# Performance work log

Measured on AMD Instinct MI355X. Metric: run time of the kernel, lower is better.

The kernel has to match this reference:

```python
import jax, jax.numpy as jnp
import numpy as np

V, K, D, T, B, M = 32000, 32, 256, 128, 128, 16
NEG = -1e9


def setup_inputs():
    key = jax.random.key(0)
    ks = jax.random.split(key, 32)
    def rn(k, shape):
        return (0.05 * jax.random.normal(k, shape)).astype(jnp.float32)
    u = jax.random.uniform(ks[4], (T, B, K), minval=1e-6, maxval=1.0 - 1e-6)
    return dict(
        keys=jax.random.randint(ks[0], (B, M), 1, V),
        vals=jax.random.randint(ks[1], (B, M), 1, V),
        sentences=jax.random.randint(ks[2], (B, T), 1, V),
        sent_lens=jax.random.randint(ks[3], (B,), T // 2, T + 1),
        tau=jnp.float32(0.5),
        x_lambd=jnp.float32(0.5),
        gumbel_noise=(-jnp.log(-jnp.log(u))).astype(jnp.float32),
        drop_unif=jax.random.uniform(ks[5], (B, T)).astype(jnp.float32),
        emb=rn(ks[6], (V, D)), z_emb=rn(ks[7], (K, D)),
        enc_Wih=rn(ks[8], (D, 4 * D)), enc_Whh=rn(ks[9], (D, 4 * D)), enc_b=jnp.zeros((4 * D,), jnp.float32),
        crf_W=rn(ks[10], (D, K)), crf_b=jnp.zeros((K,), jnp.float32), crf_trans=rn(ks[11], (K, K)),
        init_Wh=rn(ks[12], (D, D)), init_bh=jnp.zeros((D,), jnp.float32),
        init_Wc=rn(ks[13], (D, D)), init_bc=jnp.zeros((D,), jnp.float32),
        dec_Wih=rn(ks[14], (D, 4 * D)), dec_Whh=rn(ks[15], (D, 4 * D)), dec_b=jnp.zeros((4 * D,), jnp.float32),
        attn_Wq=rn(ks[16], (D, D)), attn_Wk=rn(ks[17], (D, D)), attn_v=rn(ks[18], (D,)),
        attn_out_W=rn(ks[19], (2 * D, D)), attn_out_b=jnp.zeros((D,), jnp.float32),
        pz_W=rn(ks[20], (D, K)), pz_b=jnp.zeros((K,), jnp.float32),
        int_W=rn(ks[21], (2 * D, D)), int_b=jnp.zeros((D,), jnp.float32),
        out_W=rn(ks[22], (D, V)), out_b=jnp.zeros((V,), jnp.float32),
        cattn_Wq=rn(ks[23], (D, D)), cattn_Wk=rn(ks[24], (D, D)), cattn_v=rn(ks[25], (D,)),
        g_W=rn(ks[26], (D, 1)), g_b=jnp.zeros((1,), jnp.float32),
    )


def _lstm_step(h, c, x, Wih, Whh, b):
    g = x @ Wih + h @ Whh + b
    i, f, gg, o = jnp.split(g, 4, axis=-1)
    c = jax.nn.sigmoid(f) * c + jax.nn.sigmoid(i) * jnp.tanh(gg)
    h = jax.nn.sigmoid(o) * jnp.tanh(c)
    return h, c


def _attend(q, memk, mem_vals, mask, v):
    # additive attention: q [B,D], memk = mem @ Wk [B,M,D]
    e = jnp.einsum('bmd,d->bm', jnp.tanh(q[:, None, :] + memk), v)
    e = jnp.where(mask, e, NEG)
    a = jax.nn.softmax(e, axis=-1)
    ctx = jnp.einsum('bm,bmd->bd', a, mem_vals)
    return ctx, a


def _forward(tau, x_lambd, gumbel_noise, drop_unif, emb, z_emb,
             enc_Wih, enc_Whh, enc_b, crf_W, crf_b, crf_trans,
             init_Wh, init_bh, init_Wc, init_bc,
             dec_Wih, dec_Whh, dec_b,
             attn_Wq, attn_Wk, attn_v, attn_out_W, attn_out_b,
             pz_W, pz_b, int_W, int_b, out_W, out_b,
             cattn_Wq, cattn_Wk, cattn_v, g_W, g_b,
             keys, vals, sentences, sent_lens):
    z_beta = 1.0
    lens = sent_lens
    # ---- q encoder: 1-layer LSTM over sentence embeddings ----
    sent_emb = emb[sentences]                            # [B,T,D]
    def enc_step(carry, x_t):
        h, c = _lstm_step(carry[0], carry[1], x_t, enc_Wih, enc_Whh, enc_b)
        return (h, c), h
    z0 = jnp.zeros((B, D), jnp.float32)
    _, enc_out = jax.lax.scan(enc_step, (z0, z0), sent_emb.transpose(1, 0, 2))
    enc_out = enc_out.transpose(1, 0, 2)                 # [B,T,D]
    # ---- emission scores with overlap logits ----
    phi = enc_out @ crf_W + crf_b                        # [B,T,K]
    phi = phi.at[:, :-1].add(phi[:, 1:])                 # scores[:,:-1] += scores[:,1:].clone()
    phi = phi.at[:, 1:].add(phi[:, :-1])                 # scores[:,1:]  += scores[:,:-1].clone()
    # ---- linear-chain CRF forward recursion: alpha + exact entropy ----
    phiT = phi.transpose(1, 0, 2)                        # [T,B,K]
    def crf_step(carry, inputs):
        alpha, H = carry
        phi_t, t = inputs
        scores = alpha[:, :, None] + crf_trans[None]     # [B,Ki,Kj]
        lZ = jax.nn.logsumexp(scores, axis=1)            # [B,Kj]
        logw = scores - lZ[:, None, :]
        w = jnp.exp(logw)
        na = lZ + phi_t
        nH = jnp.sum(w * (H[:, :, None] - logw), axis=1)
        m = (t < lens)[:, None]
        na = jnp.where(m, na, alpha)
        nH = jnp.where(m, nH, H)
        return (na, nH), na
    (aT, HT), alphas = jax.lax.scan(
        crf_step, (phiT[0], jnp.zeros((B, K), jnp.float32)),
        (phiT[1:], jnp.arange(1, T)))
    alphas = jnp.concatenate([phiT[0][None], alphas], axis=0)   # [T,B,K]
    logp_last = jax.nn.log_softmax(aT, axis=-1)
    ent_z = jnp.mean(jnp.sum(jnp.exp(logp_last) * (HT - logp_last), axis=-1))
    # ---- Gumbel FFBS backward sampling ----
    def bwd_step(nid, inputs):
        alpha_t, g_t, t = inputs
        is_last = (t == lens - 1)[:, None]
        active = (t < lens)
        logits = jnp.where(is_last, alpha_t, alpha_t + crf_trans[:, nid].T)
        y = jax.nn.softmax((logits + g_t) / tau, axis=-1)
        y = jnp.where(active[:, None], y, 0.0)
        ids = jnp.where(active, jnp.argmax(y, axis=-1).astype(jnp.int32), 0)
        return ids, (ids, y)
    ts = jnp.arange(T)
    _, (ids_r, y_r) = jax.lax.scan(
        bwd_step, jnp.zeros((B,), jnp.int32),
        (alphas[::-1], gumbel_noise[::-1], ts[::-1]))
    z_ids = ids_r[::-1].transpose(1, 0)                  # [B,T]
    z_sample = y_r[::-1].transpose(1, 0, 2)              # [B,T,K]
    z_sample_emb = z_sample @ z_emb                      # soft gumbel encode [B,T,D]
    # ---- key-value table encoding ----
    kv_mask = keys != 0
    kv_emb = emb[keys] + emb[vals]                       # [B,M,D]
    kvm = kv_mask.astype(jnp.float32)
    kv_enc = (kv_emb * kvm[..., None]).sum(1) / kvm.sum(1, keepdims=True)
    # ---- decoder io (word dropout x_lambd, z[0] zeroed) ----
    zse = z_sample_emb.at[:, 0].multiply(0.0)
    wmask = (drop_unif > x_lambd).astype(jnp.float32)[..., None]
    dec_inputs = (zse + sent_emb * wmask)[:, :-1]        # [B,T-1,D]
    tgt_x = sentences[:, 1:]
    tgt_z = z_ids[:, 1:]
    z_next = z_sample_emb[:, 1:]
    h0 = kv_enc @ init_Wh + init_bh
    c0 = kv_enc @ init_Wc + init_bc
    memk = kv_emb @ attn_Wk
    memk2 = kv_emb @ cattn_Wk
    rows = jnp.arange(B)
    def dec_step(carry, inputs):
        h, c = carry
        x_t, zn_t, tx, tz = inputs
        h, c = _lstm_step(h, c, x_t, dec_Wih, dec_Whh, dec_b)
        ctx, _ = _attend(h @ attn_Wq, memk, kv_emb, kv_mask, attn_v)
        dec_out = jnp.concatenate([h, ctx], axis=-1) @ attn_out_W + attn_out_b
        z_logits = dec_out @ pz_W + pz_b
        lpz = jnp.take_along_axis(jax.nn.log_softmax(z_logits, -1), tz[:, None], 1)[:, 0]
        dec_int = jnp.concatenate([dec_out, zn_t], axis=-1) @ int_W + int_b
        lm_prob = jax.nn.softmax(dec_int @ out_W + out_b, axis=-1)       # [B,V]
        _, copy_dist = _attend(dec_int @ cattn_Wq, memk2, kv_emb, kv_mask, cattn_v)
        copy_prob = jnp.zeros((B, V), lm_prob.dtype).at[rows[:, None], keys].add(copy_dist)
        g = jax.nn.sigmoid(dec_int @ g_W + g_b)                           # [B,1]
        out_prob = (1.0 - g) * lm_prob + g * copy_prob
        lpx = jnp.log(jnp.take_along_axis(out_prob, tx[:, None], 1)[:, 0] + 1e-10)
        return (h, c), (lpx, lpz)
    _, (lpx, lpz) = jax.lax.scan(
        dec_step, (h0, c0),
        (dec_inputs.transpose(1, 0, 2), z_next.transpose(1, 0, 2),
         tgt_x.transpose(1, 0), tgt_z.transpose(1, 0)))
    steps = jnp.arange(T - 1)
    smask = (steps[None, :] < lens[:, None]).astype(jnp.float32)
    denom = jnp.sum(lens).astype(jnp.float32)
    p_log_prob = (jnp.sum(lpx.transpose(1, 0) * smask) + jnp.sum(lpz.transpose(1, 0) * smask)) / denom
    loss = -(z_beta * ent_z + p_log_prob)
    return loss


def reference(keys, vals, sentences, sent_lens, tau, x_lambd, gumbel_noise,
              drop_unif, emb, z_emb, enc_Wih, enc_Whh, enc_b, crf_W, crf_b,
              crf_trans, init_Wh, init_bh, init_Wc, init_bc, dec_Wih, dec_Whh,
              dec_b, attn_Wq, attn_Wk, attn_v, attn_out_W, attn_out_b, pz_W,
              pz_b, int_W, int_b, out_W, out_b, cattn_Wq, cattn_Wk, cattn_v,
              g_W, g_b):
    return _forward(tau, x_lambd, gumbel_noise, drop_unif, emb, z_emb,
                    enc_Wih, enc_Whh, enc_b, crf_W, crf_b, crf_trans,
                    init_Wh, init_bh, init_Wc, init_bc, dec_Wih, dec_Whh,
                    dec_b, attn_Wq, attn_Wk, attn_v, attn_out_W, attn_out_b,
                    pz_W, pz_b, int_W, int_b, out_W, out_b,
                    cattn_Wq, cattn_Wk, cattn_v, g_W, g_b,
                    keys, vals, sentences, sent_lens)
```

## Files before the change

kernel.cpp:

```cpp
#include <hip/hip_runtime.h>
#include <math.h>

namespace {

constexpr int V_  = 32000;
constexpr int K_  = 32;
constexpr int D_  = 256;
constexpr int T_  = 128;
constexpr int B_  = 128;
constexpr int M_  = 16;
constexpr int D4_ = 1024;
constexpr int TD_ = T_ - 1;
constexpr int R_  = B_ * TD_;
constexpr int NCH_ = 8;

typedef __attribute__((ext_vector_type(8))) short short8;
typedef __attribute__((ext_vector_type(4))) float f32x4;
typedef __attribute__((ext_vector_type(2))) float f32x2;

__device__ __forceinline__ float d_rcp(float x){
#if __has_builtin(__builtin_amdgcn_rcpf)
  return __builtin_amdgcn_rcpf(x);
#else
  return 1.0f / x;
#endif
}
__device__ __forceinline__ float d_sig(float x){
  return d_rcp(1.0f + __expf(-x));
}
__device__ __forceinline__ float d_tanh(float x){
  float e = __expf(2.0f*x);
  return 1.0f - 2.0f*d_rcp(e + 1.0f);
}
__device__ __forceinline__ unsigned short f2bf(float f){
  unsigned int x = __float_as_uint(f);
  unsigned int r = (x + 0x7FFFu + ((x>>16)&1u)) >> 16;
  return (unsigned short)r;
}

__device__ __forceinline__ unsigned f2fp8(float f){
  unsigned u = __float_as_uint(f);
  unsigned s = (u>>31)<<7;
  float a = fabsf(f);
  if (a < 0.015625f){
    int m = (int)rintf(a*512.0f);
    if (m >= 8) return s | 0x08u;
    return s | (unsigned)m;
  }
  unsigned t = u & 0x7FFFFFFFu;
  t += 0x7FFFFu + ((t>>20)&1u);
  int E = (int)(t>>23) - 127 + 7;
  if (E >= 16) return s | 0x7Eu;
  return s | ((unsigned)E<<3) | ((t>>20)&7u);
}

__device__ __forceinline__ unsigned pack4_fp8(float a, float b, float c, float d){
#if __has_builtin(__builtin_amdgcn_cvt_pk_fp8_f32)
  unsigned r = (unsigned)__builtin_amdgcn_cvt_pk_fp8_f32(a, b, 0, false);
  r = (unsigned)__builtin_amdgcn_cvt_pk_fp8_f32(c, d, (int)r, true);
  return r;
#else
  return f2fp8(a) | (f2fp8(b)<<8) | (f2fp8(c)<<16) | (f2fp8(d)<<24);
#endif
}
__device__ __forceinline__ unsigned char f2fp8_b(float f){
#if __has_builtin(__builtin_amdgcn_cvt_pk_fp8_f32)
  return (unsigned char)(__builtin_amdgcn_cvt_pk_fp8_f32(f, f, 0, false) & 0xFF);
#else
  return (unsigned char)f2fp8(f);
#endif
}

__device__ __forceinline__ void cvt4_fp8(unsigned w, float* o){
#if __has_builtin(__builtin_amdgcn_cvt_pk_f32_fp8)
  f32x2 lo = __builtin_amdgcn_cvt_pk_f32_fp8(w, false);
  f32x2 hi = __builtin_amdgcn_cvt_pk_f32_fp8(w, true);
  o[0]=lo.x; o[1]=lo.y; o[2]=hi.x; o[3]=hi.y;
#else
  #pragma unroll
  for (int j = 0; j < 4; j++){
    unsigned b = (w>>(8*j)) & 0xFFu;
    unsigned e = (b>>3) & 15u, m = b & 7u;
    float mag = e ? __uint_as_float(((e+120u)<<23)|(m<<20)) : (float)m*0.001953125f;
    o[j] = (b & 0x80u) ? -mag : mag;
  }
#endif
}

__global__ void k_emb2(const int* __restrict__ sent, const int* __restrict__ keys,
                       const int* __restrict__ vals, const float* __restrict__ emb,
                       float* __restrict__ sent_emb, float* __restrict__ kv){
  int bid = blockIdx.x, tid = threadIdx.x;
  if (bid < B_*T_){
    sent_emb[(size_t)bid*256 + tid] = emb[(size_t)sent[bid]*D_ + tid];
  } else {
    int r = bid - B_*T_;
    kv[(size_t)r*256 + tid] = emb[(size_t)keys[r]*D_ + tid]
                            + emb[(size_t)vals[r]*D_ + tid];
  }
}

__global__ void k_kv_enc(const int* __restrict__ keys, const float* __restrict__ kv,
                         float* __restrict__ out){
  int idx = blockIdx.x*256 + threadIdx.x;
  int b = idx >> 8, d = idx & 255;
  float s = 0.0f, c = 0.0f;
  for (int m = 0; m < M_; m++){
    if (keys[b*M_+m] != 0){ s += kv[(size_t)(b*M_+m)*D_ + d]; c += 1.0f; }
  }
  out[idx] = s / c;
}

__global__ void k_rowgemm(const float* __restrict__ A, const float* __restrict__ W,
                          const float* __restrict__ bias, float* __restrict__ C,
                          int inner, int cols){
  __shared__ float sA[256];
  int r = blockIdx.x;
  if ((int)threadIdx.x < inner) sA[threadIdx.x] = A[(size_t)r*inner + threadIdx.x];
  __syncthreads();
  for (int j = threadIdx.x; j < cols; j += blockDim.x){
    float acc = bias ? bias[j] : 0.0f;
    #pragma unroll 4
    for (int d = 0; d < inner; d++) acc += sA[d]*W[(size_t)d*cols + j];
    C[(size_t)r*cols + j] = acc;
  }
}

__global__ void k_rowgemm2(const float* __restrict__ A,
                           const float* __restrict__ W1, const float* __restrict__ b1,
                           float* __restrict__ C1,
                           const float* __restrict__ W2, const float* __restrict__ b2,
                           float* __restrict__ C2, int inner, int cols){
  __shared__ float sA[256];
  int r = blockIdx.x;
  if ((int)threadIdx.x < inner) sA[threadIdx.x] = A[(size_t)r*inner + threadIdx.x];
  __syncthreads();
  for (int j = threadIdx.x; j < cols; j += blockDim.x){
    float a1 = b1 ? b1[j] : 0.0f;
    float a2 = b2 ? b2[j] : 0.0f;
    #pragma unroll 4
    for (int d = 0; d < inner; d++){
      float a = sA[d];
      a1 += a*W1[(size_t)d*cols + j];
      a2 += a*W2[(size_t)d*cols + j];
    }
    C1[(size_t)r*cols + j] = a1;
    C2[(size_t)r*cols + j] = a2;
  }
}

__global__ __launch_bounds__(256) void k_wt8(const float* __restrict__ W,
                                             unsigned char* __restrict__ Wt8, int ldw){
  __shared__ unsigned char st[64][272];
  int tid = threadIdx.x; size_t c0 = (size_t)blockIdx.x*64;
  for (int l = tid; l < 64*256; l += 256){
    int k = l >> 6, c = l & 63;
    st[c][k] = f2fp8_b(W[(size_t)k*ldw + c0 + c]);
  }
  __syncthreads();
  for (int l = tid; l < 64*16; l += 256){
    int c = l >> 4, s = l & 15;
    *reinterpret_cast<uint4*>(&Wt8[(c0+c)*256 + s*16]) =
      *reinterpret_cast<const uint4*>(&st[c][s*16]);
  }
}

__global__ __launch_bounds__(256) void k_wt8_2(const float* __restrict__ W1,
    const float* __restrict__ W2, unsigned char* __restrict__ O1,
    unsigned char* __restrict__ O2, int ldw){
  __shared__ unsigned char st[64][272];
  const float* W = (blockIdx.x < 16) ? W1 : W2;
  unsigned char* O = (blockIdx.x < 16) ? O1 : O2;
  int tid = threadIdx.x; size_t c0 = (size_t)(blockIdx.x & 15)*64;
  for (int l = tid; l < 64*256; l += 256){
    int k = l >> 6, c = l & 63;
    st[c][k] = f2fp8_b(W[(size_t)k*ldw + c0 + c]);
  }
  __syncthreads();
  for (int l = tid; l < 64*16; l += 256){
    int c = l >> 4, s = l & 15;
    *reinterpret_cast<uint4*>(&O[(c0+c)*256 + s*16]) =
      *reinterpret_cast<const uint4*>(&st[c][s*16]);
  }
}

__global__ __launch_bounds__(256) void k_wtg2(const float* __restrict__ W1,
    const float* __restrict__ W2, unsigned short* __restrict__ O1,
    unsigned short* __restrict__ O2, int ldw){
  __shared__ unsigned short st[64][264];
  const float* W = (blockIdx.x < 16) ? W1 : W2;
  unsigned short* O = (blockIdx.x < 16) ? O1 : O2;
  int tid = threadIdx.x; size_t c0 = (size_t)(blockIdx.x & 15)*64;
  for (int l = tid; l < 64*256; l += 256){
    int k = l >> 6, c = l & 63;
    st[c][k] = f2bf(W[(size_t)k*ldw + c0 + c]);
  }
  __syncthreads();
  for (int l = tid; l < 64*32; l += 256){
    int c = l >> 5, s = l & 31;
    *reinterpret_cast<uint4*>(&O[(c0+c)*256 + s*8]) =
      *reinterpret_cast<const uint4*>(&st[c][s*8]);
  }
}

__global__ __launch_bounds__(256) void k_wtg6(
    const float* s0, const float* s1, const float* s2,
    const float* s3, const float* s4, const float* s5,
    unsigned short* d0, unsigned short* d1, unsigned short* d2,
    unsigned short* d3, unsigned short* d4, unsigned short* d5){
  __shared__ unsigned short st[64][264];
  int m = blockIdx.x >> 2, blk = blockIdx.x & 3;
  const float* S; unsigned short* D;
  if      (m == 0){ S = s0; D = d0; }
  else if (m == 1){ S = s1; D = d1; }
  else if (m == 2){ S = s2; D = d2; }
  else if (m == 3){ S = s3; D = d3; }
  else if (m == 4){ S = s4; D = d4; }
  else            { S = s5; D = d5; }
  int tid = threadIdx.x; size_t c0 = (size_t)blk*64;
  for (int l = tid; l < 64*256; l += 256){
    int k = l >> 6, c = l & 63;
    st[c][k] = f2bf(S[(size_t)k*256 + c0 + c]);
  }
  __syncthreads();
  for (int l = tid; l < 64*32; l += 256){
    int c = l >> 5, s = l & 31;
    *reinterpret_cast<uint4*>(&D[(c0+c)*256 + s*8]) =
      *reinterpret_cast<const uint4*>(&st[c][s*8]);
  }
}

template<int G1, int G2, int HALVES, int CPB, bool BIAS, int TMD>
__global__ __launch_bounds__(512) void k_gemm(
    const float* __restrict__ A1, const float* __restrict__ A2,
    const unsigned short* __restrict__ W1, const unsigned short* __restrict__ W2,
    const float* __restrict__ bias, float* __restrict__ C, int cols,
    const float* __restrict__ drop, const float* __restrict__ xl){
  __shared__ unsigned short Al[128*256];
  __shared__ unsigned short Wl[64*256];
  int tid = threadIdx.x;
  int row0 = blockIdx.x*128;
  int w = tid >> 6, l = tid & 63;
  int arow = 16*w + (l & 15);
  float xlv = 0.0f;
  if constexpr (G1==1) xlv = xl[0];
  f32x4 acc[CPB][4];
  #pragma unroll
  for (int cc=0;cc<CPB;cc++)
    #pragma unroll
    for (int nf=0;nf<4;nf++) acc[cc][nf] = (f32x4){0.f,0.f,0.f,0.f};

  for (int h = 0; h < HALVES; h++){
    const float* Asrc = h ? A2 : A1;
    const unsigned short* Wt = h ? W2 : W1;
    int gm = h ? G2 : G1;
    __syncthreads();
    #pragma unroll
    for (int q = 0; q < 8; q++){
      int u = tid + q*512;
      int row = u >> 5, slot = u & 31;
      int r = row0 + row;
      float vals[8];
      if (gm == 0){
        const float* s = Asrc + (size_t)r*256 + slot*8;
        #pragma unroll
        for (int j=0;j<8;j++) vals[j] = s[j];
      } else if (gm == 1){
        int b = r / TD_, t = r - b*TD_;
        int bt = b*T_ + t;
        float wm = (drop[bt] > xlv) ? 1.0f : 0.0f;
        const float* se = A1 + (size_t)bt*256 + slot*8;
        const float* zs = A2 + (size_t)bt*256 + slot*8;
        #pragma unroll
        for (int j=0;j<8;j++) vals[j] = se[j]*wm + (t>0 ? zs[j] : 0.0f);
      } else {
        int b = r / TD_, t = r - b*TD_;
        const float* s = Asrc + (size_t)(b*T_ + t + 1)*256 + slot*8;
        #pragma unroll
        for (int j=0;j<8;j++) vals[j] = s[j];
      }
      union { unsigned short us[8]; uint4 v4; } tu;
      #pragma unroll
      for (int j=0;j<8;j++) tu.us[j] = f2bf(vals[j]);
      int dst = row*512 + ((slot*16) ^ ((row&7)<<4));
      *reinterpret_cast<uint4*>(reinterpret_cast<char*>(Al) + dst) = tu.v4;
    }
    __syncthreads();
    short8 afr[8];
    #pragma unroll
    for (int k0 = 0; k0 < 8; k0++){
      int kb = k0*64 + ((l>>4)*16);
      afr[k0] = *reinterpret_cast<const short8*>(
          reinterpret_cast<const char*>(Al) + arow*512 + (kb ^ ((arow&7)<<4)));
    }
    for (int cc = 0; cc < CPB; cc++){
      int col0 = (blockIdx.y*CPB + cc)*64;
      __syncthreads();
      #pragma unroll
      for (int q = 0; q < 4; q++){
        int u = tid + q*512;
        int c = u >> 5, slot = u & 31;
        int dst = c*512 + ((slot*16) ^ ((c&7)<<4));
        *reinterpret_cast<uint4*>(reinterpret_cast<char*>(Wl) + dst) =
          *reinterpret_cast<const uint4*>(
              reinterpret_cast<const char*>(Wt) + (size_t)(col0+c)*512 + slot*16);
      }
      __syncthreads();
      #pragma unroll
      for (int k0 = 0; k0 < 8; k0++){
        int kb = k0*64 + ((l>>4)*16);
        #pragma unroll
        for (int nf = 0; nf < 4; nf++){
          int bc = nf*16 + (l & 15);
          short8 bfr = *reinterpret_cast<const short8*>(
              reinterpret_cast<const char*>(Wl) + bc*512 + (kb ^ ((bc&7)<<4)));
          acc[cc][nf] = __builtin_amdgcn_mfma_f32_16x16x32_bf16(afr[k0], bfr, acc[cc][nf], 0, 0, 0);
        }
      }
    }
  }
  #pragma unroll
  for (int cc = 0; cc < CPB; cc++){
    int col0 = (blockIdx.y*CPB + cc)*64;
    #pragma unroll
    for (int nf = 0; nf < 4; nf++){
      int col = col0 + nf*16 + (l & 15);
      float bv = BIAS ? bias[col] : 0.0f;
      #pragma unroll
      for (int r4 = 0; r4 < 4; r4++){
        int row = row0 + 16*w + (l>>4)*4 + r4;
        size_t orow;
        if constexpr (TMD == 0){
          orow = (size_t)row;
        } else {
          int bb = row / TMD, tt = row - bb*TMD;
          orow = (size_t)tt*B_ + bb;
        }
        C[orow*cols + col] = acc[cc][nf][r4] + bv;
      }
    }
  }
}

__global__ __launch_bounds__(1024, 4) void k_lstm12(
    const float* __restrict__ xW,
    const unsigned char* __restrict__ Wt,
    const float* __restrict__ h0, const float* __restrict__ c0,
    float* __restrict__ Hout,
    int NT){
  __shared__ unsigned char Wl[512*256];
  __shared__ unsigned char Ahl[2][16*256];
  int g0 = blockIdx.x;
  int tid = threadIdx.x;
  int w = tid >> 6, l = tid & 63;

  for (int i = tid; i < 512*16; i += 1024){
    int c = i >> 4, s16 = i & 15;
    int dst = c*256 + ((s16*16) ^ ((c&7)<<4));
    *reinterpret_cast<uint4*>(&Wl[dst]) =
      *reinterpret_cast<const uint4*>(&Wt[(size_t)c*256 + s16*16]);
  }
  if (tid < 256){
    int row = tid >> 4, gblk = tid & 15;
    unsigned pk[4];
    #pragma unroll
    for (int g = 0; g < 4; g++){
      float v0 = h0 ? h0[(size_t)(g0*16+row)*256 + gblk*16 + 4*g + 0] : 0.0f;
      float v1 = h0 ? h0[(size_t)(g0*16+row)*256 + gblk*16 + 4*g + 1] : 0.0f;
      float v2 = h0 ? h0[(size_t)(g0*16+row)*256 + gblk*16 + 4*g + 2] : 0.0f;
      float v3 = h0 ? h0[(size_t)(g0*16+row)*256 + gblk*16 + 4*g + 3] : 0.0f;
      pk[g] = pack4_fp8(v0, v1, v2, v3);
    }
    int dst = row*256 + ((gblk*16) ^ ((row&7)<<4));
    *reinterpret_cast<uint4*>(&Ahl[0][dst]) = *reinterpret_cast<const uint4*>(pk);
  }
  int cb = 16*w + (l & 15);
  int arow = l & 15;
  float creg[4];
  #pragma unroll
  for (int r = 0; r < 4; r++)
    creg[r] = c0 ? c0[(size_t)(g0*16 + (l>>4)*4 + r)*256 + cb] : 0.0f;

  int aoff[8], b0off[8], b1off[8];
  #pragma unroll
  for (int k0 = 0; k0 < 8; k0++){
    int kb = k0*32 + ((l>>4)*8);
    aoff[k0]  = arow*256 + (kb ^ ((arow&7)<<4));
    b0off[k0] = cb*256 + (kb ^ ((cb&7)<<4));
    b1off[k0] = (256+cb)*256 + (kb ^ ((cb&7)<<4));
  }
  const unsigned char* wg2 = Wt + (size_t)(512+cb)*256 + ((l>>4)*8);
  const unsigned char* wg3 = Wt + (size_t)(768+cb)*256 + ((l>>4)*8);
  int astore[4];
  const float* xb[4];
  float* hp[4];
  #pragma unroll
  for (int r = 0; r < 4; r++){
    int batch = (l>>4)*4 + r;
    astore[r] = batch*256 + ((cb & 0xF0) ^ ((batch&7)<<4)) + (cb & 15);
    xb[r] = xW + (size_t)(g0*16 + batch)*1024 + cb;
    hp[r] = Hout + (size_t)(g0*16 + batch)*NT*256 + cb;
  }
  __syncthreads();

  float xn[4][4];
  #pragma unroll
  for (int gt = 0; gt < 4; gt++)
    #pragma unroll
    for (int r = 0; r < 4; r++)
      xn[gt][r] = xb[r][gt*256];

  for (int t = 0; t < NT; t++){
    int cur = t & 1, nxt = cur ^ 1;
    f32x4 acc[4];
    #pragma unroll
    for (int gt = 0; gt < 4; gt++)
      #pragma unroll
      for (int r = 0; r < 4; r++)
        acc[gt][r] = xn[gt][r];
    if (t + 1 < NT){
      #pragma unroll
      for (int r = 0; r < 4; r++) xb[r] += B_*1024;
      #pragma unroll
      for (int gt = 0; gt < 4; gt++)
        #pragma unroll
        for (int r = 0; r < 4; r++)
          xn[gt][r] = xb[r][gt*256];
    }
    const unsigned char* Ac = Ahl[cur];
    #pragma unroll
    for (int k0 = 0; k0 < 8; k0++){
      long long afr = *reinterpret_cast<const long long*>(Ac + aoff[k0]);
      long long b0 = *reinterpret_cast<const long long*>(Wl + b0off[k0]);
      long long b1 = *reinterpret_cast<const long long*>(Wl + b1off[k0]);
      long long b2 = *reinterpret_cast<const long long*>(wg2 + k0*32);
      long long b3 = *reinterpret_cast<const long long*>(wg3 + k0*32);
      acc[0] = __builtin_amdgcn_mfma_f32_16x16x32_fp8_fp8(afr, b0, acc[0], 0, 0, 0);
      acc[1] = __builtin_amdgcn_mfma_f32_16x16x32_fp8_fp8(afr, b1, acc[1], 0, 0, 0);
      acc[2] = __builtin_amdgcn_mfma_f32_16x16x32_fp8_fp8(afr, b2, acc[2], 0, 0, 0);
      acc[3] = __builtin_amdgcn_mfma_f32_16x16x32_fp8_fp8(afr, b3, acc[3], 0, 0, 0);
    }
    #pragma unroll
    for (int r = 0; r < 4; r++){
      float vi = acc[0][r], vf = acc[1][r];
      float vg = acc[2][r], vo = acc[3][r];
      float cn = d_sig(vf)*creg[r] + d_sig(vi)*d_tanh(vg);
      float hn = d_sig(vo)*d_tanh(cn);
      creg[r] = cn;
      Ahl[nxt][astore[r]] = f2fp8_b(hn);
      hp[r][0] = hn;
      hp[r] += 256;
    }
    __syncthreads();
  }
}

__global__ __launch_bounds__(256) void k_phi(const float* __restrict__ H,
    const float* __restrict__ Wc, const float* __restrict__ bc,
    float* __restrict__ phi){
  int tid = threadIdx.x; int rl = tid >> 5, j = tid & 31;
  int r = blockIdx.x*8 + rl;
  int b = r >> 7, t = r & 127;
  float acc = bc[j];
  #pragma unroll 4
  for (int d = 0; d < 256; d++) acc += H[(size_t)r*256 + d]*Wc[d*K_ + j];
  phi[(size_t)t*B_*K_ + b*K_ + j] = acc;
}

__global__ __launch_bounds__(256) void k_zlp(const float* __restrict__ A,
    const float* __restrict__ Wz, const float* __restrict__ bz,
    const int* __restrict__ zids, float* __restrict__ lpz){
  int tid = threadIdx.x; int rl = tid >> 5, j = tid & 31;
  int r = blockIdx.x*8 + rl;
  float acc = bz[j];
  #pragma unroll 4
  for (int d = 0; d < 256; d++) acc += A[(size_t)r*256 + d]*Wz[d*K_ + j];
  float m = acc;
  #pragma unroll
  for (int off=16; off; off>>=1) m = fmaxf(m, __shfl_xor(m, off, 32));
  float e = __expf(acc - m), E = e;
  #pragma unroll
  for (int off=16; off; off>>=1) E += __shfl_xor(E, off, 32);
  int b = r / TD_, t = r - b*TD_;
  int tz = zids[b*T_ + t + 1];
  float vtz = __shfl(acc, tz, 32);
  if (j == 0) lpz[r] = vtz - (m + logf(E));
}

__global__ __launch_bounds__(1024) void k_crf(
    const float* __restrict__ phi, const float* __restrict__ trans,
    const int* __restrict__ lens, float* __restrict__ alphas,
    float* __restrict__ ent_b){
  __shared__ float sal[2][K_], sH[2][K_];
  int tid = threadIdx.x, b = blockIdx.x;
  int i = tid & 31, j = tid >> 5;
  float tr = trans[i*K_ + j];
  int len = lens[b];
  if (tid < K_){
    float a0 = phi[b*K_ + tid] + phi[(size_t)B_*K_ + b*K_ + tid];
    sal[0][tid] = a0; sH[0][tid] = 0.0f;
    alphas[b*K_ + tid] = a0;
  }
  __syncthreads();
  for (int t = 1; t < T_; t++){
    int cur = (t-1) & 1, nxt = t & 1;
    bool active = (t < len);
    float ai = sal[cur][i], Hi = sH[cur][i];
    float aj = sal[cur][j], Hj = sH[cur][j];
    float s = ai + tr;
    float m = s;
    #pragma unroll
    for (int off=16; off; off>>=1) m = fmaxf(m, __shfl_xor(m, off, 32));
    float e = expf(s - m);
    float E = e;
    #pragma unroll
    for (int off=16; off; off>>=1) E += __shfl_xor(E, off, 32);
    float lZ = m + logf(E);
    float w = e / E;
    float logw = s - lZ;
    float nH = w * (Hi - logw);
    #pragma unroll
    for (int off=16; off; off>>=1) nH += __shfl_xor(nH, off, 32);
    float pm = phi[(size_t)(t-1)*B_*K_ + b*K_ + j];
    float pt = phi[(size_t)t*B_*K_ + b*K_ + j];
    float ps = (t == T_-1) ? (pm + 2.0f*pt)
                           : (pm + 2.0f*pt + phi[(size_t)(t+1)*B_*K_ + b*K_ + j]);
    float na = lZ + ps;
    float outa = active ? na : aj;
    float outH = active ? nH : Hj;
    if (i == 0){
      sal[nxt][j] = outa; sH[nxt][j] = outH;
      alphas[(size_t)t*B_*K_ + b*K_ + j] = outa;
    }
    __syncthreads();
  }
  int fb = (T_-1) & 1;
  if (tid < K_){
    float a = sal[fb][tid];
    float m = a;
    #pragma unroll
    for (int off=16; off; off>>=1) m = fmaxf(m, __shfl_xor(m, off, 32));
    float e = expf(a-m), E = e;
    #pragma unroll
    for (int off=16; off; off>>=1) E += __shfl_xor(E, off, 32);
    float lse = m + logf(E);
    float lp = a - lse;
    float v = expf(lp)*(sH[fb][tid]-lp);
    #pragma unroll
    for (int off=16; off; off>>=1) v += __shfl_xor(v, off, 32);
    if (tid == 0) ent_b[b] = v;
  }
}

__global__ void k_sampler(const float* __restrict__ alphas, const float* __restrict__ trans,
                          const float* __restrict__ gum, const int* __restrict__ lens,
                          const float* __restrict__ tau_p,
                          float* __restrict__ y_all, int* __restrict__ z_ids){
  int b = blockIdx.x;
  int lane = threadIdx.x;
  int k = lane & 31;
  float inv_tau = d_rcp(tau_p[0]);
  int len = lens[b];
  int nid = 0;
  for (int t = T_-1; t >= 0; t--){
    bool active  = (t < len);
    bool is_last = (t == len-1);
    float a = alphas[(size_t)t*B_*K_ + b*K_ + k];
    float lg = is_last ? a : a + trans[k*K_ + nid];
    float val = (lg + gum[(size_t)t*B_*K_ + b*K_ + k]) * inv_tau;
    float m = val;
    #pragma unroll
    for (int off=16; off; off>>=1) m = fmaxf(m, __shfl_xor(m, off, 32));
    float e = expf(val - m), E = e;
    #pragma unroll
    for (int off=16; off; off>>=1) E += __shfl_xor(E, off, 32);
    float y = active ? e*d_rcp(E) : 0.0f;
    if (lane < K_) y_all[(size_t)(b*T_ + t)*K_ + k] = y;
    float bv = val; int bk = k;
    #pragma unroll
    for (int off=16; off; off>>=1){
      float ov = __shfl_xor(bv, off, 32);
      int   ok = __shfl_xor(bk, off, 32);
      if (ov > bv || (ov == bv && ok < bk)){ bv = ov; bk = ok; }
    }
    int ids = active ? bk : 0;
    nid = ids;
    if (lane == 0) z_ids[b*T_ + t] = ids;
  }
}

__global__ __launch_bounds__(256) void k_attn1(
    const float* __restrict__ q, const float* __restrict__ memk,
    const float* __restrict__ kv_emb, const int* __restrict__ keys,
    const float* __restrict__ av, float* __restrict__ ctx){
  __shared__ float se[16];
  int r = blockIdx.x, tid = threadIdx.x;
  int b = r / TD_;
  int m = tid >> 4, ds = tid & 15;
  float p = 0.0f;
  #pragma unroll 4
  for (int qq = 0; qq < 16; qq++){
    int dd = ds + qq*16;
    p += d_tanh(q[(size_t)r*256 + dd] + memk[(size_t)(b*M_+m)*256 + dd]) * av[dd];
  }
  #pragma unroll
  for (int off=8; off; off>>=1) p += __shfl_xor(p, off, 16);
  if (ds == 0) se[m] = (keys[b*M_+m] != 0) ? p : -1e9f;
  __syncthreads();
  float mx = -1e30f;
  #pragma unroll
  for (int mm=0;mm<16;mm++) mx = fmaxf(mx, se[mm]);
  float den = 0.0f, ex[16];
  #pragma unroll
  for (int mm=0;mm<16;mm++){ ex[mm] = __expf(se[mm]-mx); den += ex[mm]; }
  float cacc = 0.0f;
  #pragma unroll
  for (int mm=0;mm<16;mm++) cacc += ex[mm]*kv_emb[(size_t)(b*M_+mm)*256 + tid];
  ctx[(size_t)r*256 + tid] = cacc*d_rcp(den);
}

__global__ __launch_bounds__(256) void k_attn2g(
    const float* __restrict__ q2, const float* __restrict__ dint,
    const float* __restrict__ memk2, const int* __restrict__ keys,
    const float* __restrict__ cv, const float* __restrict__ gW, const float* __restrict__ gb,
    const int* __restrict__ sent,
    float* __restrict__ cpx, float* __restrict__ gsig){
  __shared__ float se2[16];
  __shared__ float sred[4];
  int r = blockIdx.x, tid = threadIdx.x;
  int b = r / TD_, t = r - b*TD_;
  int m = tid >> 4, ds = tid & 15;
  float p = 0.0f;
  #pragma unroll 4
  for (int qq = 0; qq < 16; qq++){
    int dd = ds + qq*16;
    p += d_tanh(q2[(size_t)r*256 + dd] + memk2[(size_t)(b*M_+m)*256 + dd]) * cv[dd];
  }
  #pragma unroll
  for (int off=8; off; off>>=1) p += __shfl_xor(p, off, 16);
  if (ds == 0) se2[m] = (keys[b*M_+m] != 0) ? p : -1e9f;
  float gp = dint[(size_t)r*256 + tid]*gW[tid];
  #pragma unroll
  for (int off=32; off; off>>=1) gp += __shfl_xor(gp, off, 64);
  if ((tid & 63) == 0) sred[tid>>6] = gp;
  __syncthreads();
  if (tid == 0){
    float mx = -1e30f;
    #pragma unroll
    for (int mm=0;mm<16;mm++) mx = fmaxf(mx, se2[mm]);
    float den = 0.0f, ex[16];
    #pragma unroll
    for (int mm=0;mm<16;mm++){ ex[mm] = __expf(se2[mm]-mx); den += ex[mm]; }
    int txi = sent[b*T_ + t + 1];
    float idn = d_rcp(den);
    float cp = 0.0f;
    #pragma unroll
    for (int mm=0;mm<16;mm++) if (keys[b*M_+mm] == txi) cp += ex[mm]*idn;
    cpx[r] = cp;
    gsig[r] = d_sig(sred[0]+sred[1]+sred[2]+sred[3] + gb[0]);
  }
}

__global__ __launch_bounds__(512) void k_lse8(
    const float* __restrict__ Af,
    const unsigned char* __restrict__ Wt8,
    const float* __restrict__ bias,
    float* __restrict__ part){
  __shared__ unsigned char Al[256*256];
  __shared__ unsigned char Wl[64*256];
  int tid = threadIdx.x;
  int row0 = blockIdx.x*256;
  #pragma unroll
  for (int q = 0; q < 8; q++){
    int u = tid + q*512;
    int row = u >> 4, s16 = u & 15;
    int r = row0 + row;
    unsigned pk[4] = {0u,0u,0u,0u};
    if (r < R_){
      const float* src = Af + (size_t)r*256 + s16*16;
      #pragma unroll
      for (int g = 0; g < 4; g++){
        float4 f = *reinterpret_cast<const float4*>(src + g*4);
        pk[g] = pack4_fp8(f.x, f.y, f.z, f.w);
      }
    }
    int dst = row*256 + ((s16*16) ^ ((row&7)<<4));
    *reinterpret_cast<uint4*>(&Al[dst]) = *reinterpret_cast<const uint4*>(pk);
  }
  __syncthreads();
  int w = tid >> 6, l = tid & 63;
  int arow = 16*w + (l & 15);
  long long afrA[8], afrB[8];
  #pragma unroll
  for (int k0 = 0; k0 < 8; k0++){
    int kb = k0*32 + ((l>>4)*8);
    afrA[k0] = *reinterpret_cast<const long long*>(&Al[arow*256 + (kb ^ ((arow&7)<<4))]);
    int ar2 = arow + 128;
    afrB[k0] = *reinterpret_cast<const long long*>(&Al[ar2*256 + (kb ^ ((ar2&7)<<4))]);
  }
  float rm[2][4], rs[2][4];
  #pragma unroll
  for (int rf=0;rf<2;rf++)
    #pragma unroll
    for (int r4=0;r4<4;r4++){ rm[rf][r4] = -3.0e38f; rs[rf][r4] = 0.0f; }

  for (int ct = blockIdx.y; ct < 500; ct += NCH_){
    int col0 = ct*64;
    __syncthreads();
    #pragma unroll
    for (int q = 0; q < 2; q++){
      int u = tid + q*512;
      int c = u >> 4, s16 = u & 15;
      int dst = c*256 + ((s16*16) ^ ((c&7)<<4));
      *reinterpret_cast<uint4*>(&Wl[dst]) =
        *reinterpret_cast<const uint4*>(&Wt8[(size_t)(col0+c)*256 + s16*16]);
    }
    __syncthreads();
    f32x4 acc[2][4];
    #pragma unroll
    for (int rf=0;rf<2;rf++)
      #pragma unroll
      for (int nf=0;nf<4;nf++) acc[rf][nf] = (f32x4){0.f,0.f,0.f,0.f};
    #pragma unroll
    for (int k0 = 0; k0 < 8; k0++){
      int kb = k0*32 + ((l>>4)*8);
      #pragma unroll
      for (int nf = 0; nf < 4; nf++){
        int bc = nf*16 + (l & 15);
        long long bfr = *reinterpret_cast<const long long*>(&Wl[bc*256 + (kb ^ ((bc&7)<<4))]);
        acc[0][nf] = __builtin_amdgcn_mfma_f32_16x16x32_fp8_fp8(afrA[k0], bfr, acc[0][nf], 0, 0, 0);
        acc[1][nf] = __builtin_amdgcn_mfma_f32_16x16x32_fp8_fp8(afrB[k0], bfr, acc[1][nf], 0, 0, 0);
      }
    }
    float bb[4];
    #pragma unroll
    for (int nf=0;nf<4;nf++) bb[nf] = bias[col0 + nf*16 + (l&15)];
    #pragma unroll
    for (int rf = 0; rf < 2; rf++){
      #pragma unroll
      for (int r4 = 0; r4 < 4; r4++){
        float v0 = acc[rf][0][r4]+bb[0], v1 = acc[rf][1][r4]+bb[1];
        float v2 = acc[rf][2][r4]+bb[2], v3 = acc[rf][3][r4]+bb[3];
        float tm = fmaxf(fmaxf(v0,v1), fmaxf(v2,v3));
        float ts = __expf(v0-tm)+__expf(v1-tm)+__expf(v2-tm)+__expf(v3-tm);
        float m0 = rm[rf][r4];
        if (tm <= m0){
          rs[rf][r4] += ts*__expf(tm - m0);
        } else {
          rs[rf][r4] = rs[rf][r4]*__expf(m0 - tm) + ts;
          rm[rf][r4] = tm;
        }
      }
    }
  }
  #pragma unroll
  for (int rf = 0; rf < 2; rf++){
    #pragma unroll
    for (int r4 = 0; r4 < 4; r4++){
      float M = rm[rf][r4];
      #pragma unroll
      for (int off=8; off; off>>=1) M = fmaxf(M, __shfl_xor(M, off, 16));
      float S = rs[rf][r4]*__expf(rm[rf][r4] - M);
      #pragma unroll
      for (int off=8; off; off>>=1) S += __shfl_xor(S, off, 16);
      if ((l & 15) == 0){
        int grow = row0 + rf*128 + 16*w + (l>>4)*4 + r4;
        if (grow < R_){
          part[((size_t)grow*NCH_ + blockIdx.y)*2 + 0] = M;
          part[((size_t)grow*NCH_ + blockIdx.y)*2 + 1] = S;
        }
      }
    }
  }
}

__global__ void k_lse_combine(const float* __restrict__ part, float* __restrict__ lse){
  int r = blockIdx.x*256 + threadIdx.x;
  if (r >= R_) return;
  float M = -3.0e38f;
  for (int c = 0; c < NCH_; c++) M = fmaxf(M, part[((size_t)r*NCH_+c)*2]);
  float S = 0.0f;
  for (int c = 0; c < NCH_; c++){
    float m = part[((size_t)r*NCH_+c)*2], s = part[((size_t)r*NCH_+c)*2+1];
    S += s*__expf(m - M);
  }
  lse[r] = M + logf(S);
}

__global__ __launch_bounds__(256) void k_ltx(const float* __restrict__ dint,
    const unsigned char* __restrict__ Wt8, const float* __restrict__ bias,
    const int* __restrict__ sent, float* __restrict__ out){
  int tid = threadIdx.x;
  int r = blockIdx.x*4 + (tid >> 6);
  int lane = tid & 63;
  int b = r / TD_, t = r - b*TD_;
  int tx = sent[b*T_ + t + 1];
  unsigned wq = *reinterpret_cast<const unsigned*>(Wt8 + (size_t)tx*256 + lane*4);
  float wv[4]; cvt4_fp8(wq, wv);
  const float* ap = dint + (size_t)r*256 + lane*4;
  unsigned aq = pack4_fp8(ap[0], ap[1], ap[2], ap[3]);
  float av[4]; cvt4_fp8(aq, av);
  float acc = av[0]*wv[0] + av[1]*wv[1] + av[2]*wv[2] + av[3]*wv[3];
  #pragma unroll
  for (int off=32; off; off>>=1) acc += __shfl_xor(acc, off, 64);
  if (lane == 0) out[r] = acc + bias[tx];
}

__global__ __launch_bounds__(256) void k_final(
    const float* __restrict__ lse, const float* __restrict__ ltx,
    const float* __restrict__ gsig, const float* __restrict__ cpx,
    const float* __restrict__ lpz, const float* __restrict__ ent_b,
    const int* __restrict__ lens, float* __restrict__ out){
  __shared__ float sred[256];
  int tid = threadIdx.x;
  float sum = 0.0f;
  for (int r = tid; r < R_; r += 256){
    int b = r / TD_, t = r % TD_;
    if (t < lens[b]){
      float g = gsig[r];
      float lm = __expf(ltx[r] - lse[r]);
      float p = (1.0f-g)*lm + g*cpx[r] + 1e-10f;
      sum += logf(p) + lpz[r];
    }
  }
  sred[tid] = sum;
  __syncthreads();
  for (int s = 128; s; s >>= 1){ if (tid < s) sred[tid] += sred[tid+s]; __syncthreads(); }
  if (tid == 0){
    float es = 0.0f, dn = 0.0f;
    for (int b = 0; b < B_; b++){ es += ent_b[b]; dn += (float)lens[b]; }
    out[0] = -( es/(float)B_ + sred[0]/dn );
  }
}

}

extern "C" void kernel_launch(void* const* d_in, const int* in_sizes, int n_in,
                              void* d_out, int out_size, void* d_ws, size_t ws_size,
                              hipStream_t stream){
  const int*   keys  = (const int*)d_in[0];
  const int*   vals  = (const int*)d_in[1];
  const int*   sent  = (const int*)d_in[2];
  const int*   lens  = (const int*)d_in[3];
  const float* tau   = (const float*)d_in[4];
  const float* xl    = (const float*)d_in[5];
  const float* gum   = (const float*)d_in[6];
  const float* drop  = (const float*)d_in[7];
  const float* emb   = (const float*)d_in[8];
  const float* z_emb = (const float*)d_in[9];
  const float* eWih  = (const float*)d_in[10];
  const float* eWhh  = (const float*)d_in[11];
  const float* eb    = (const float*)d_in[12];
  const float* crfW  = (const float*)d_in[13];
  const float* crfb  = (const float*)d_in[14];
  const float* trans = (const float*)d_in[15];
  const float* iWh   = (const float*)d_in[16];
  const float* ibh   = (const float*)d_in[17];
  const float* iWc   = (const float*)d_in[18];
  const float* ibc   = (const float*)d_in[19];
  const float* dWih  = (const float*)d_in[20];
  const float* dWhh  = (const float*)d_in[21];
  const float* db    = (const float*)d_in[22];
  const float* aWq   = (const float*)d_in[23];
  const float* aWk   = (const float*)d_in[24];
  const float* av    = (const float*)d_in[25];
  const float* aoW   = (const float*)d_in[26];
  const float* aob   = (const float*)d_in[27];
  const float* pzW   = (const float*)d_in[28];
  const float* pzb   = (const float*)d_in[29];
  const float* intW  = (const float*)d_in[30];
  const float* intb  = (const float*)d_in[31];
  const float* outW  = (const float*)d_in[32];
  const float* outb  = (const float*)d_in[33];
  const float* cWq   = (const float*)d_in[34];
  const float* cWk   = (const float*)d_in[35];
  const float* cv    = (const float*)d_in[36];
  const float* gW    = (const float*)d_in[37];
  const float* gb    = (const float*)d_in[38];
  (void)in_sizes; (void)n_in; (void)out_size; (void)ws_size;

  float* ws = (float*)d_ws;
  size_t o = 0;
  auto alloc = [&](size_t n){ size_t r = o; o += (n + 3) & ~(size_t)3; return r; };
  float* sent_emb = ws + alloc((size_t)B_*T_*D_);
  float* kv_emb   = ws + alloc((size_t)B_*M_*D_);
  float* kv_enc   = ws + alloc((size_t)B_*D_);
  float* h0       = ws + alloc((size_t)B_*D_);
  float* c0       = ws + alloc((size_t)B_*D_);
  float* memk     = ws + alloc((size_t)B_*M_*D_);
  float* memk2    = ws + alloc((size_t)B_*M_*D_);
  float* xW       = ws + alloc((size_t)B_*T_*D4_);
  float* encH     = ws + alloc((size_t)B_*T_*D_);
  float* phi_raw  = ws + alloc((size_t)T_*B_*K_);
  float* alphas   = ws + alloc((size_t)T_*B_*K_);
  float* ent_b    = ws + alloc((size_t)B_);
  float* y_all    = ws + alloc((size_t)B_*T_*K_);
  float* zse      = ws + alloc((size_t)B_*T_*D_);
  float* qbuf     = ws + alloc((size_t)R_*D_);
  float* ctx      = ws + alloc((size_t)R_*D_);
  float* dec_out  = ws + alloc((size_t)R_*D_);
  float* dint     = ws + alloc((size_t)R_*D_);
  float* lpz_b    = ws + alloc((size_t)R_);
  float* gsig     = ws + alloc((size_t)R_);
  float* cpx      = ws + alloc((size_t)R_);
  float* ltx      = ws + alloc((size_t)R_);
  float* lse      = ws + alloc((size_t)R_);
  float* part     = ws + alloc((size_t)R_*NCH_*2);
  int*   z_ids    = (int*)(ws + alloc((size_t)B_*T_));
  unsigned char* WhhT8E = (unsigned char*)(ws + alloc((size_t)D4_*D_/4));
  unsigned char* WhhT8D = (unsigned char*)(ws + alloc((size_t)D4_*D_/4));
  unsigned char* Wt8    = (unsigned char*)(ws + alloc((size_t)V_*D_/4));
  unsigned short* eWihT = (unsigned short*)(ws + alloc((size_t)D4_*D_/2));
  unsigned short* dWihT = (unsigned short*)(ws + alloc((size_t)D4_*D_/2));
  unsigned short* aWqT  = (unsigned short*)(ws + alloc((size_t)D_*D_/2));
  unsigned short* cWqT  = (unsigned short*)(ws + alloc((size_t)D_*D_/2));
  unsigned short* aoWtT = (unsigned short*)(ws + alloc((size_t)D_*D_/2));
  unsigned short* aoWbT = (unsigned short*)(ws + alloc((size_t)D_*D_/2));
  unsigned short* inWtT = (unsigned short*)(ws + alloc((size_t)D_*D_/2));
  unsigned short* inWbT = (unsigned short*)(ws + alloc((size_t)D_*D_/2));

  float* Hdec = encH;

  k_emb2<<<B_*T_ + B_*M_, 256, 0, stream>>>(sent, keys, vals, emb, sent_emb, kv_emb);
  k_kv_enc<<<B_*D_/256, 256, 0, stream>>>(keys, kv_emb, kv_enc);
  k_rowgemm2<<<B_, 256, 0, stream>>>(kv_enc, iWh, ibh, h0, iWc, ibc, c0, 256, 256);
  k_rowgemm2<<<B_*M_, 256, 0, stream>>>(kv_emb, aWk, nullptr, memk,
                                        cWk, nullptr, memk2, 256, 256);
  k_wt8_2<<<32, 256, 0, stream>>>(eWhh, dWhh, WhhT8E, WhhT8D, D4_);
  k_wt8<<<V_/64, 256, 0, stream>>>(outW, Wt8, V_);
  k_wtg2<<<32, 256, 0, stream>>>(eWih, dWih, eWihT, dWihT, D4_);
  k_wtg6<<<24, 256, 0, stream>>>(aWq, cWq, aoW, aoW + 256*256, intW, intW + 256*256,
                                 aWqT, cWqT, aoWtT, aoWbT, inWtT, inWbT);

  k_gemm<0,0,1,4,true,T_><<<dim3(B_*T_/128, 4), 512, 0, stream>>>(
      sent_emb, nullptr, eWihT, nullptr, eb, xW, D4_, nullptr, nullptr);
  k_lstm12<<<B_/16, 1024, 0, stream>>>(xW, WhhT8E, nullptr, nullptr, encH, T_);
  k_phi<<<B_*T_/8, 256, 0, stream>>>(encH, crfW, crfb, phi_raw);
  k_crf<<<B_, 1024, 0, stream>>>(phi_raw, trans, lens, alphas, ent_b);
  k_sampler<<<B_, 64, 0, stream>>>(alphas, trans, gum, lens, tau, y_all, z_ids);
  k_rowgemm<<<B_*T_, 256, 0, stream>>>(y_all, z_emb, nullptr, zse, K_, 256);

  k_gemm<1,0,1,4,true,TD_><<<dim3(R_/128, 4), 512, 0, stream>>>(
      sent_emb, zse, dWihT, nullptr, db, xW, D4_, drop, xl);
  k_lstm12<<<B_/16, 1024, 0, stream>>>(xW, WhhT8D, h0, c0, Hdec, TD_);

  k_gemm<0,0,1,1,false,0><<<dim3(R_/128, 4), 512, 0, stream>>>(
      Hdec, nullptr, aWqT, nullptr, nullptr, qbuf, D_, nullptr, nullptr);
  k_attn1<<<R_, 256, 0, stream>>>(qbuf, memk, kv_emb, keys, av, ctx);
  k_gemm<0,0,2,1,true,0><<<dim3(R_/128, 4), 512, 0, stream>>>(
      Hdec, ctx, aoWtT, aoWbT, aob, dec_out, D_, nullptr, nullptr);
  k_zlp<<<R_/8, 256, 0, stream>>>(dec_out, pzW, pzb, z_ids, lpz_b);
  k_gemm<0,2,2,1,true,0><<<dim3(R_/128, 4), 512, 0, stream>>>(
      dec_out, zse, inWtT, inWbT, intb, dint, D_, nullptr, nullptr);
  k_gemm<0,0,1,1,false,0><<<dim3(R_/128, 4), 512, 0, stream>>>(
      dint, nullptr, cWqT, nullptr, nullptr, qbuf, D_, nullptr, nullptr);
  k_attn2g<<<R_, 256, 0, stream>>>(qbuf, dint, memk2, keys, cv, gW, gb, sent,
                                   cpx, gsig);

  k_lse8<<<dim3((R_+255)/256, NCH_), 512, 0, stream>>>(dint, Wt8, outb, part);
  k_lse_combine<<<(R_+255)/256, 256, 0, stream>>>(part, lse);
  k_ltx<<<R_/4, 256, 0, stream>>>(dint, Wt8, outb, sent, ltx);
  k_final<<<1, 256, 0, stream>>>(lse, ltx, gsig, cpx, lpz_b, ent_b, lens, (float*)d_out);
}
```

Before: 1.742 ms.

## Tile LSTM input layout, stage rows in LDS, precompute fp8 activations once

The input-projection GEMM now writes the time-major xW buffer in a tiled layout, so each LSTM lane fetches its four gate values for four batches as contiguous float4 loads instead of sixteen scattered scalars per step. k_phi and k_zlp stage their 8 rows into shared memory with vector loads rather than each thread re-reading global memory. A new k_a8 kernel converts dint to fp8 once, and both k_lse8 (eight grid-y chunks) and k_ltx reuse it instead of repacking from fp32. This adds an extra kernel launch and buffer, and the tiled layout must match the GEMM write indexing exactly.

```diff
diff --git a/kernel.cpp b/kernel.cpp
--- a/kernel.cpp
+++ b/kernel.cpp
@@ -329,14 +329,16 @@
       #pragma unroll
       for (int r4 = 0; r4 < 4; r4++){
         int row = row0 + 16*w + (l>>4)*4 + r4;
-        size_t orow;
+        float v = acc[cc][nf][r4] + bv;
         if constexpr (TMD == 0){
-          orow = (size_t)row;
+          C[(size_t)row*cols + col] = v;
         } else {
           int bb = row / TMD, tt = row - bb*TMD;
-          orow = (size_t)tt*B_ + bb;
+          int gt = col >> 8, cbx = col & 255;
+          size_t off = (((size_t)tt*8 + (bb>>4))*256 + cbx)*64
+                     + ((bb&15)>>2)*16 + gt*4 + (bb&3);
+          C[off] = v;
         }
-        C[orow*cols + col] = acc[cc][nf][r4] + bv;
       }
     }
   }
@@ -392,40 +394,31 @@
   const unsigned char* wg2 = Wt + (size_t)(512+cb)*256 + ((l>>4)*8);
   const unsigned char* wg3 = Wt + (size_t)(768+cb)*256 + ((l>>4)*8);
   int astore[4];
-  const float* xb[4];
   float* hp[4];
   #pragma unroll
   for (int r = 0; r < 4; r++){
     int batch = (l>>4)*4 + r;
     astore[r] = batch*256 + ((cb & 0xF0) ^ ((batch&7)<<4)) + (cb & 15);
-    xb[r] = xW + (size_t)(g0*16 + batch)*1024 + cb;
     hp[r] = Hout + (size_t)(g0*16 + batch)*NT*256 + cb;
   }
-  __syncthreads();
-
-  float xn[4][4];
+  const float* xb = xW + ((size_t)g0*256 + cb)*64 + (l>>4)*16;
+  __syncthreads();
+
+  f32x4 xn[4];
   #pragma unroll
   for (int gt = 0; gt < 4; gt++)
-    #pragma unroll
-    for (int r = 0; r < 4; r++)
-      xn[gt][r] = xb[r][gt*256];
+    xn[gt] = *reinterpret_cast<const f32x4*>(xb + gt*4);
 
   for (int t = 0; t < NT; t++){
     int cur = t & 1, nxt = cur ^ 1;
     f32x4 acc[4];
     #pragma unroll
-    for (int gt = 0; gt < 4; gt++)
-      #pragma unroll
-      for (int r = 0; r < 4; r++)
-        acc[gt][r] = xn[gt][r];
+    for (int gt = 0; gt < 4; gt++) acc[gt] = xn[gt];
     if (t + 1 < NT){
-      #pragma unroll
-      for (int r = 0; r < 4; r++) xb[r] += B_*1024;
+      xb += 8*16384;
       #pragma unroll
       for (int gt = 0; gt < 4; gt++)
-        #pragma unroll
-        for (int r = 0; r < 4; r++)
-          xn[gt][r] = xb[r][gt*256];
+        xn[gt] = *reinterpret_cast<const f32x4*>(xb + gt*4);
     }
     const unsigned char* Ac = Ahl[cur];
     #pragma unroll
@@ -458,23 +451,39 @@
 __global__ __launch_bounds__(256) void k_phi(const float* __restrict__ H,
     const float* __restrict__ Wc, const float* __restrict__ bc,
     float* __restrict__ phi){
+  __shared__ float sH[8][256];
   int tid = threadIdx.x; int rl = tid >> 5, j = tid & 31;
-  int r = blockIdx.x*8 + rl;
+  int r0 = blockIdx.x*8;
+  for (int i = tid; i < 512; i += 256){
+    int rr = i >> 6, c4 = i & 63;
+    *reinterpret_cast<float4*>(&sH[rr][c4*4]) =
+      *reinterpret_cast<const float4*>(&H[(size_t)(r0+rr)*256 + c4*4]);
+  }
+  __syncthreads();
+  int r = r0 + rl;
   int b = r >> 7, t = r & 127;
   float acc = bc[j];
   #pragma unroll 4
-  for (int d = 0; d < 256; d++) acc += H[(size_t)r*256 + d]*Wc[d*K_ + j];
+  for (int d = 0; d < 256; d++) acc += sH[rl][d]*Wc[d*K_ + j];
   phi[(size_t)t*B_*K_ + b*K_ + j] = acc;
 }
 
 __global__ __launch_bounds__(256) void k_zlp(const float* __restrict__ A,
     const float* __restrict__ Wz, const float* __restrict__ bz,
     const int* __restrict__ zids, float* __restrict__ lpz){
+  __shared__ float sA[8][256];
   int tid = threadIdx.x; int rl = tid >> 5, j = tid & 31;
-  int r = blockIdx.x*8 + rl;
+  int r0 = blockIdx.x*8;
+  for (int i = tid; i < 512; i += 256){
+    int rr = i >> 6, c4 = i & 63;
+    *reinterpret_cast<float4*>(&sA[rr][c4*4]) =
+      *reinterpret_cast<const float4*>(&A[(size_t)(r0+rr)*256 + c4*4]);
+  }
+  __syncthreads();
+  int r = r0 + rl;
   float acc = bz[j];
   #pragma unroll 4
-  for (int d = 0; d < 256; d++) acc += A[(size_t)r*256 + d]*Wz[d*K_ + j];
+  for (int d = 0; d < 256; d++) acc += sA[rl][d]*Wz[d*K_ + j];
   float m = acc;
   #pragma unroll
   for (int off=16; off; off>>=1) m = fmaxf(m, __shfl_xor(m, off, 32));
@@ -661,8 +670,15 @@
   }
 }
 
+__global__ void k_a8(const float* __restrict__ dint, unsigned* __restrict__ A8){
+  int idx = blockIdx.x*256 + threadIdx.x;
+  if (idx >= R_*64) return;
+  float4 f = *reinterpret_cast<const float4*>(dint + (size_t)idx*4);
+  A8[idx] = pack4_fp8(f.x, f.y, f.z, f.w);
+}
+
 __global__ __launch_bounds__(512) void k_lse8(
-    const float* __restrict__ Af,
+    const unsigned char* __restrict__ A8,
     const unsigned char* __restrict__ Wt8,
     const float* __restrict__ bias,
     float* __restrict__ part){
@@ -675,17 +691,11 @@
     int u = tid + q*512;
     int row = u >> 4, s16 = u & 15;
     int r = row0 + row;
-    unsigned pk[4] = {0u,0u,0u,0u};
-    if (r < R_){
-      const float* src = Af + (size_t)r*256 + s16*16;
-      #pragma unroll
-      for (int g = 0; g < 4; g++){
-        float4 f = *reinterpret_cast<const float4*>(src + g*4);
-        pk[g] = pack4_fp8(f.x, f.y, f.z, f.w);
-      }
-    }
+    uint4 pk = (uint4){0u,0u,0u,0u};
+    if (r < R_)
+      pk = *reinterpret_cast<const uint4*>(A8 + (size_t)r*256 + s16*16);
     int dst = row*256 + ((s16*16) ^ ((row&7)<<4));
-    *reinterpret_cast<uint4*>(&Al[dst]) = *reinterpret_cast<const uint4*>(pk);
+    *reinterpret_cast<uint4*>(&Al[dst]) = pk;
   }
   __syncthreads();
   int w = tid >> 6, l = tid & 63;
@@ -787,7 +797,7 @@
   lse[r] = M + logf(S);
 }
 
-__global__ __launch_bounds__(256) void k_ltx(const float* __restrict__ dint,
+__global__ __launch_bounds__(256) void k_ltx(const unsigned char* __restrict__ A8,
     const unsigned char* __restrict__ Wt8, const float* __restrict__ bias,
     const int* __restrict__ sent, float* __restrict__ out){
   int tid = threadIdx.x;
@@ -797,8 +807,7 @@
   int tx = sent[b*T_ + t + 1];
   unsigned wq = *reinterpret_cast<const unsigned*>(Wt8 + (size_t)tx*256 + lane*4);
   float wv[4]; cvt4_fp8(wq, wv);
-  const float* ap = dint + (size_t)r*256 + lane*4;
-  unsigned aq = pack4_fp8(ap[0], ap[1], ap[2], ap[3]);
+  unsigned aq = *reinterpret_cast<const unsigned*>(A8 + (size_t)r*256 + lane*4);
   float av[4]; cvt4_fp8(aq, av);
   float acc = av[0]*wv[0] + av[1]*wv[1] + av[2]*wv[2] + av[3]*wv[3];
   #pragma unroll
@@ -907,6 +916,7 @@
   float* lse      = ws + alloc((size_t)R_);
   float* part     = ws + alloc((size_t)R_*NCH_*2);
   int*   z_ids    = (int*)(ws + alloc((size_t)B_*T_));
+  unsigned* A8    = (unsigned*)(ws + alloc((size_t)R_*64));
   unsigned char* WhhT8E = (unsigned char*)(ws + alloc((size_t)D4_*D_/4));
   unsigned char* WhhT8D = (unsigned char*)(ws + alloc((size_t)D4_*D_/4));
   unsigned char* Wt8    = (unsigned char*)(ws + alloc((size_t)V_*D_/4));
@@ -952,13 +962,15 @@
   k_zlp<<<R_/8, 256, 0, stream>>>(dec_out, pzW, pzb, z_ids, lpz_b);
   k_gemm<0,2,2,1,true,0><<<dim3(R_/128, 4), 512, 0, stream>>>(
       dec_out, zse, inWtT, inWbT, intb, dint, D_, nullptr, nullptr);
+  k_a8<<<(R_*64+255)/256, 256, 0, stream>>>(dint, A8);
   k_gemm<0,0,1,1,false,0><<<dim3(R_/128, 4), 512, 0, stream>>>(
       dint, nullptr, cWqT, nullptr, nullptr, qbuf, D_, nullptr, nullptr);
   k_attn2g<<<R_, 256, 0, stream>>>(qbuf, dint, memk2, keys, cv, gW, gb, sent,
                                    cpx, gsig);
 
-  k_lse8<<<dim3((R_+255)/256, NCH_), 512, 0, stream>>>(dint, Wt8, outb, part);
+  k_lse8<<<dim3((R_+255)/256, NCH_), 512, 0, stream>>>(
+      (const unsigned char*)A8, Wt8, outb, part);
   k_lse_combine<<<(R_+255)/256, 256, 0, stream>>>(part, lse);
-  k_ltx<<<R_/4, 256, 0, stream>>>(dint, Wt8, outb, sent, ltx);
+  k_ltx<<<R_/4, 256, 0, stream>>>((const unsigned char*)A8, Wt8, outb, sent, ltx);
   k_final<<<1, 256, 0, stream>>>(lse, ltx, gsig, cpx, lpz_b, ent_b, lens, (float*)d_out);
 }
```

Result: slower. 2.218 ms (+27.3%).
